# Kernel tuning notes

Measured on AMD Instinct MI355X. Metric: run time of the kernel, lower is better.

Reference implementation:

```python
import jax, jax.numpy as jnp
import numpy as np

N_NODES = 100000


def gcn_layer(x, row, col, ew, W, b, n_nodes):
    # PyG GCNConv: add self-loops (weight 1), symmetric normalization
    # deg^{-1/2}[row] * w * deg^{-1/2}[col], linear transform, scatter-add to col.
    loop = jnp.arange(n_nodes, dtype=row.dtype)
    row_f = jnp.concatenate([row, loop])
    col_f = jnp.concatenate([col, loop])
    ew_f = jnp.concatenate([ew, jnp.ones((n_nodes,), dtype=ew.dtype)])
    deg = jax.ops.segment_sum(ew_f, col_f, num_segments=n_nodes)  # [N]
    dinv = jnp.where(deg > 0, jax.lax.rsqrt(deg), 0.0)
    norm = dinv[row_f] * ew_f * dinv[col_f]  # [E+N]
    h = x @ W  # [N, F_out]
    msg = norm[:, None] * h[row_f]  # [E+N, F_out]
    out = jax.ops.segment_sum(msg, col_f, num_segments=n_nodes)
    return out + b


def setup_inputs() -> dict:
    key = jax.random.key(0)
    ks = jax.random.split(key, 6)
    n, e, d_in, d_h = N_NODES, 3200000, 128, 16
    x = jax.random.normal(ks[0], (n, d_in), dtype=jnp.float32)
    edge_index = jax.random.randint(ks[1], (2, e), 0, n, dtype=jnp.int64)
    edge_weight = jax.random.uniform(ks[2], (e,), dtype=jnp.float32)
    W1 = jax.random.normal(ks[3], (d_in, d_h), dtype=jnp.float32) * (1.0 / np.sqrt(d_in))
    b1 = jnp.zeros((d_h,), dtype=jnp.float32)
    W2 = jax.random.normal(ks[4], (d_h, 1), dtype=jnp.float32) * (1.0 / np.sqrt(d_h))
    b2 = jnp.zeros((1,), dtype=jnp.float32)
    return {"x": x, "edge_index": edge_index, "edge_weight": edge_weight,
            "W1": W1, "b1": b1, "W2": W2, "b2": b2}


def reference(x, edge_index, edge_weight, W1, b1, W2, b2):
    row, col = edge_index[0], edge_index[1]
    n = x.shape[0]
    h = gcn_layer(x, row, col, edge_weight, W1, b1, n)
    h = jax.nn.relu(h)
    out = gcn_layer(h, row, col, edge_weight, W2, b2, n)
    return out.squeeze(-1)  # [N]
```

## Files before the change

### kernel.cpp

```cpp
#include <hip/hip_runtime.h>


#define DH 16

__global__ void k_hist(const int* __restrict__ col, int* __restrict__ cnt, int E) {
    int e = blockIdx.x * blockDim.x + threadIdx.x;
    if (e < E) atomicAdd(&cnt[col[e]], 1);
}

__global__ __launch_bounds__(256) void k_scan1(const int* __restrict__ cnt,
                                               int* __restrict__ rowptr,
                                               int* __restrict__ blocksum, int N) {
    __shared__ int s[256];
    int i = blockIdx.x * 256 + threadIdx.x;
    int v = (i < N) ? cnt[i] : 0;
    s[threadIdx.x] = v;
    __syncthreads();
    for (int off = 1; off < 256; off <<= 1) {
        int t = (threadIdx.x >= off) ? s[threadIdx.x - off] : 0;
        __syncthreads();
        s[threadIdx.x] += t;
        __syncthreads();
    }
    if (i < N) rowptr[i] = s[threadIdx.x];
    if (threadIdx.x == 255) blocksum[blockIdx.x] = s[255];
}

__global__ __launch_bounds__(512) void k_scan2(int* __restrict__ blocksum, int nb) {
    __shared__ int s[512];
    int t = threadIdx.x;
    int v = (t < nb) ? blocksum[t] : 0;
    s[t] = v;
    __syncthreads();
    for (int off = 1; off < 512; off <<= 1) {
        int u = (t >= off) ? s[t - off] : 0;
        __syncthreads();
        s[t] += u;
        __syncthreads();
    }
    if (t < nb) blocksum[t] = s[t] - v;
}

__global__ void k_scan3(const int* __restrict__ cnt, int* __restrict__ rowptr,
                        const int* __restrict__ blocksum, int* __restrict__ cursor,
                        int N, int E) {
    int i = blockIdx.x * 256 + threadIdx.x;
    if (i < N) {
        int ex = blocksum[blockIdx.x] + rowptr[i] - cnt[i];
        rowptr[i] = ex;
        cursor[i] = ex;
    }
    if (i == 0) rowptr[N] = E;
}

__global__ void k_scatter(const int* __restrict__ row, const int* __restrict__ col,
                          const float* __restrict__ ew, int* __restrict__ cursor,
                          uint2* __restrict__ edata, int E) {
    int e = blockIdx.x * blockDim.x + threadIdx.x;
    if (e >= E) return;
    int slot = atomicAdd(&cursor[col[e]], 1);
    edata[slot] = make_uint2((unsigned)row[e], __float_as_uint(ew[e]));
}

__global__ __launch_bounds__(256) void k_degcsr(const int* __restrict__ rowptr,
                                                const uint2* __restrict__ edata,
                                                float* __restrict__ dinv, int N) {
    int node = (blockIdx.x * 256 + threadIdx.x) >> 6;
    if (node >= N) return;
    int lane = threadIdx.x & 63;
    int base = rowptr[node], end = rowptr[node + 1];
    float s = 0.f;
    for (int i = base + lane; i < end; i += 64) s += __uint_as_float(edata[i].y);
    #pragma unroll
    for (int m = 1; m < 64; m <<= 1) s += __shfl_xor(s, m, 64);
    if (lane == 0) dinv[node] = rsqrtf(s + 1.0f);
}

__global__ __launch_bounds__(256) void k_h1(const float* __restrict__ x,
                                            const float* __restrict__ W1,
                                            float* __restrict__ h) {
    __shared__ float Ws[128 * DH];
    __shared__ float xs[16 * 132];
    const int t = threadIdx.x;
    const int node0 = blockIdx.x * 16;

    #pragma unroll
    for (int i = 0; i < 8; ++i) Ws[t + 256 * i] = W1[t + 256 * i];

    const float4* xg = (const float4*)(x + (size_t)node0 * 128);
    #pragma unroll
    for (int it = 0; it < 2; ++it) {
        int idx = t + 256 * it;
        int n = idx >> 5, k4 = idx & 31;
        float4 v = xg[n * 32 + k4];
        *(float4*)(&xs[n * 132 + k4 * 4]) = v;
    }
    __syncthreads();

    const int node = t >> 4, feat = t & 15;
    const float* xr = &xs[node * 132];
    float acc = 0.f;
    #pragma unroll 8
    for (int k = 0; k < 128; ++k) acc += xr[k] * Ws[k * DH + feat];
    h[(size_t)(node0 + node) * DH + feat] = acc;
}

__global__ __launch_bounds__(256) void k_gather1(
    const int* __restrict__ rowptr, const uint2* __restrict__ edata,
    const float* __restrict__ dinv, const float* __restrict__ h,
    const float* __restrict__ b1, const float* __restrict__ W2,
    float* __restrict__ q, int N) {
    int node = (blockIdx.x * 256 + threadIdx.x) >> 6;
    if (node >= N) return;
    int lane = threadIdx.x & 63;
    int feat = lane & 15, g = lane >> 4;
    int base = rowptr[node], end = rowptr[node + 1];
    float acc = 0.f;
    for (int i = base + g; i < end; i += 4) {
        uint2 ed = edata[i];
        int r = ed.x;
        float w = __uint_as_float(ed.y);
        acc += dinv[r] * w * h[(size_t)r * DH + feat];
    }
    acc += __shfl_xor(acc, 16, 64);
    acc += __shfl_xor(acc, 32, 64);
    float dc = dinv[node];
    float ag = dc * acc + dc * dc * h[(size_t)node * DH + feat];
    float t = fmaxf(ag + b1[feat], 0.f) * W2[feat];
    t += __shfl_xor(t, 1, 64);
    t += __shfl_xor(t, 2, 64);
    t += __shfl_xor(t, 4, 64);
    t += __shfl_xor(t, 8, 64);
    if (lane == 0) q[node] = dc * t;
}

__global__ __launch_bounds__(256) void k_gather2(
    const int* __restrict__ rowptr, const uint2* __restrict__ edata,
    const float* __restrict__ dinv, const float* __restrict__ q,
    const float* __restrict__ b2, float* __restrict__ out, int N) {
    int node = (blockIdx.x * 256 + threadIdx.x) >> 6;
    if (node >= N) return;
    int lane = threadIdx.x & 63;
    int base = rowptr[node], end = rowptr[node + 1];
    float acc = 0.f;
    for (int i = base + lane; i < end; i += 64) {
        uint2 ed = edata[i];
        acc += __uint_as_float(ed.y) * q[ed.x];
    }
    #pragma unroll
    for (int m = 1; m < 64; m <<= 1) acc += __shfl_xor(acc, m, 64);
    if (lane == 0) out[node] = b2[0] + dinv[node] * (acc + q[node]);
}

extern "C" void kernel_launch(void* const* d_in, const int* in_sizes, int n_in,
                              void* d_out, int out_size, void* d_ws, size_t ws_size,
                              hipStream_t stream) {
    const float* x  = (const float*)d_in[0];
    const int*   ei = (const int*)d_in[1];
    const float* ew = (const float*)d_in[2];
    const float* W1 = (const float*)d_in[3];
    const float* b1 = (const float*)d_in[4];
    const float* W2 = (const float*)d_in[5];
    const float* b2 = (const float*)d_in[6];
    float* out = (float*)d_out;

    const int N = in_sizes[0] / 128;
    const int E = in_sizes[2];
    const int* row = ei;
    const int* col = ei + E;

    int* cnt      = (int*)d_ws;
    int* rowptr   = cnt + N;
    int* cursor   = rowptr + N + 1;
    int* blocksum = cursor + N;
    float* dinv   = (float*)(blocksum + 512);
    float* h      = dinv + N;
    float* q      = h + (size_t)16 * N;
    uintptr_t ep  = (uintptr_t)(q + N);
    ep = (ep + 7) & ~(uintptr_t)7;
    uint2* edata  = (uint2*)ep;

    const int eb = (E + 255) / 256;
    const int G1 = (N + 255) / 256;
    const int nodeb = (N * 64 + 255) / 256;

    hipMemsetAsync(cnt, 0, (size_t)N * sizeof(int), stream);
    k_hist<<<eb, 256, 0, stream>>>(col, cnt, E);
    k_scan1<<<G1, 256, 0, stream>>>(cnt, rowptr, blocksum, N);
    k_scan2<<<1, 512, 0, stream>>>(blocksum, G1);
    k_scan3<<<G1, 256, 0, stream>>>(cnt, rowptr, blocksum, cursor, N, E);
    k_scatter<<<eb, 256, 0, stream>>>(row, col, ew, cursor, edata, E);
    k_degcsr<<<nodeb, 256, 0, stream>>>(rowptr, edata, dinv, N);
    k_h1<<<N / 16, 256, 0, stream>>>(x, W1, h);
    k_gather1<<<nodeb, 256, 0, stream>>>(rowptr, edata, dinv, h, b1, W2, q, N);
    k_gather2<<<nodeb, 256, 0, stream>>>(rowptr, edata, dinv, q, b2, out, N);
}
```

Before: 641.0 us.

## Replace per-node CSR with 128-node bucket partitioning and shared-memory accumulation

Edges are no longer sorted into an exact per-node CSR. They are bucketed by destination into groups of 128 nodes, using block-local shared-memory histograms and one global cursor atomic per bucket, with the local node index packed into the high bits of the row id. Degree and both aggregation passes then run one block per bucket and accumulate into shared memory with LDS atomics. This removes the per-edge global atomics and the multi-pass scan, but adds shared-memory atomic contention and assumes row ids fit in 20 bits and NB is at most 784.

```diff
diff --git a/kernel.cpp b/kernel.cpp
--- a/kernel.cpp
+++ b/kernel.cpp
@@ -2,78 +2,111 @@
 
 
 #define DH 16
-
-__global__ void k_hist(const int* __restrict__ col, int* __restrict__ cnt, int E) {
-    int e = blockIdx.x * blockDim.x + threadIdx.x;
-    if (e < E) atomicAdd(&cnt[col[e]], 1);
-}
-
-__global__ __launch_bounds__(256) void k_scan1(const int* __restrict__ cnt,
-                                               int* __restrict__ rowptr,
-                                               int* __restrict__ blocksum, int N) {
-    __shared__ int s[256];
-    int i = blockIdx.x * 256 + threadIdx.x;
-    int v = (i < N) ? cnt[i] : 0;
-    s[threadIdx.x] = v;
-    __syncthreads();
-    for (int off = 1; off < 256; off <<= 1) {
-        int t = (threadIdx.x >= off) ? s[threadIdx.x - off] : 0;
-        __syncthreads();
-        s[threadIdx.x] += t;
-        __syncthreads();
-    }
-    if (i < N) rowptr[i] = s[threadIdx.x];
-    if (threadIdx.x == 255) blocksum[blockIdx.x] = s[255];
-}
-
-__global__ __launch_bounds__(512) void k_scan2(int* __restrict__ blocksum, int nb) {
-    __shared__ int s[512];
-    int t = threadIdx.x;
-    int v = (t < nb) ? blocksum[t] : 0;
+#define BSH 7
+#define BNODES 128
+#define NB_MAX 784
+#define CHUNK 4096
+
+__global__ __launch_bounds__(256) void k_Ahist(const int* __restrict__ col,
+                                               int* __restrict__ gCnt, int E, int NB) {
+    __shared__ int lh[NB_MAX];
+    const int tid = threadIdx.x;
+    for (int i = tid; i < NB; i += 256) lh[i] = 0;
+    __syncthreads();
+    const int base = blockIdx.x * CHUNK;
+    #pragma unroll
+    for (int k = 0; k < 16; ++k) {
+        int e = base + tid + 256 * k;
+        if (e < E) atomicAdd(&lh[col[e] >> BSH], 1);
+    }
+    __syncthreads();
+    for (int i = tid; i < NB; i += 256) {
+        int v = lh[i];
+        if (v) atomicAdd(&gCnt[i], v);
+    }
+}
+
+__global__ __launch_bounds__(1024) void k_Ascan(const int* __restrict__ gCnt,
+                                                int* __restrict__ gBase,
+                                                int* __restrict__ gCursor,
+                                                int NB, int E) {
+    __shared__ int s[1024];
+    const int t = threadIdx.x;
+    int v = (t < NB) ? gCnt[t] : 0;
     s[t] = v;
     __syncthreads();
-    for (int off = 1; off < 512; off <<= 1) {
+    for (int off = 1; off < 1024; off <<= 1) {
         int u = (t >= off) ? s[t - off] : 0;
         __syncthreads();
         s[t] += u;
         __syncthreads();
     }
-    if (t < nb) blocksum[t] = s[t] - v;
-}
-
-__global__ void k_scan3(const int* __restrict__ cnt, int* __restrict__ rowptr,
-                        const int* __restrict__ blocksum, int* __restrict__ cursor,
-                        int N, int E) {
-    int i = blockIdx.x * 256 + threadIdx.x;
-    if (i < N) {
-        int ex = blocksum[blockIdx.x] + rowptr[i] - cnt[i];
-        rowptr[i] = ex;
-        cursor[i] = ex;
-    }
-    if (i == 0) rowptr[N] = E;
-}
-
-__global__ void k_scatter(const int* __restrict__ row, const int* __restrict__ col,
-                          const float* __restrict__ ew, int* __restrict__ cursor,
-                          uint2* __restrict__ edata, int E) {
-    int e = blockIdx.x * blockDim.x + threadIdx.x;
-    if (e >= E) return;
-    int slot = atomicAdd(&cursor[col[e]], 1);
-    edata[slot] = make_uint2((unsigned)row[e], __float_as_uint(ew[e]));
-}
-
-__global__ __launch_bounds__(256) void k_degcsr(const int* __restrict__ rowptr,
-                                                const uint2* __restrict__ edata,
-                                                float* __restrict__ dinv, int N) {
-    int node = (blockIdx.x * 256 + threadIdx.x) >> 6;
-    if (node >= N) return;
-    int lane = threadIdx.x & 63;
-    int base = rowptr[node], end = rowptr[node + 1];
-    float s = 0.f;
-    for (int i = base + lane; i < end; i += 64) s += __uint_as_float(edata[i].y);
-    #pragma unroll
-    for (int m = 1; m < 64; m <<= 1) s += __shfl_xor(s, m, 64);
-    if (lane == 0) dinv[node] = rsqrtf(s + 1.0f);
+    if (t < NB) {
+        int ex = s[t] - v;
+        gBase[t] = ex;
+        gCursor[t] = ex;
+    }
+    if (t == 0) gBase[NB] = E;
+}
+
+__global__ __launch_bounds__(256) void k_Ascatter(const int* __restrict__ row,
+                                                  const int* __restrict__ col,
+                                                  const float* __restrict__ ew,
+                                                  int* __restrict__ gCursor,
+                                                  uint2* __restrict__ edata,
+                                                  int E, int NB) {
+    __shared__ int lh[NB_MAX], lbase[NB_MAX], lcur[NB_MAX];
+    const int tid = threadIdx.x;
+    for (int i = tid; i < NB; i += 256) lh[i] = 0;
+    __syncthreads();
+    const int base = blockIdx.x * CHUNK;
+    int r_[16], c_[16];
+    float w_[16];
+    #pragma unroll
+    for (int k = 0; k < 16; ++k) {
+        int e = base + tid + 256 * k;
+        bool ok = e < E;
+        c_[k] = ok ? col[e] : -1;
+        r_[k] = ok ? row[e] : 0;
+        w_[k] = ok ? ew[e] : 0.f;
+        if (ok) atomicAdd(&lh[c_[k] >> BSH], 1);
+    }
+    __syncthreads();
+    for (int b = tid; b < NB; b += 256) {
+        int v = lh[b];
+        if (v) {
+            lbase[b] = atomicAdd(&gCursor[b], v);
+            lcur[b] = 0;
+        }
+    }
+    __syncthreads();
+    #pragma unroll
+    for (int k = 0; k < 16; ++k) {
+        if (c_[k] >= 0) {
+            int b = c_[k] >> BSH;
+            int rem = c_[k] & (BNODES - 1);
+            int off = atomicAdd(&lcur[b], 1);
+            edata[lbase[b] + off] =
+                make_uint2((unsigned)r_[k] | ((unsigned)rem << 20), __float_as_uint(w_[k]));
+        }
+    }
+}
+
+__global__ __launch_bounds__(256) void k_deg(const int* __restrict__ gBase,
+                                             const uint2* __restrict__ edata,
+                                             float* __restrict__ dinv, int N) {
+    __shared__ float dg[BNODES];
+    const int tid = threadIdx.x;
+    if (tid < BNODES) dg[tid] = 0.f;
+    __syncthreads();
+    const int s = gBase[blockIdx.x], e = gBase[blockIdx.x + 1];
+    for (int i = s + tid; i < e; i += 256) {
+        uint2 ed = edata[i];
+        atomicAdd(&dg[ed.x >> 20], __uint_as_float(ed.y));
+    }
+    __syncthreads();
+    int node = (blockIdx.x << BSH) + tid;
+    if (tid < BNODES && node < N) dinv[node] = rsqrtf(dg[tid] + 1.0f);
 }
 
 __global__ __launch_bounds__(256) void k_h1(const float* __restrict__ x,
@@ -83,10 +116,8 @@
     __shared__ float xs[16 * 132];
     const int t = threadIdx.x;
     const int node0 = blockIdx.x * 16;
-
     #pragma unroll
     for (int i = 0; i < 8; ++i) Ws[t + 256 * i] = W1[t + 256 * i];
-
     const float4* xg = (const float4*)(x + (size_t)node0 * 128);
     #pragma unroll
     for (int it = 0; it < 2; ++it) {
@@ -96,7 +127,6 @@
         *(float4*)(&xs[n * 132 + k4 * 4]) = v;
     }
     __syncthreads();
-
     const int node = t >> 4, feat = t & 15;
     const float* xr = &xs[node * 132];
     float acc = 0.f;
@@ -106,50 +136,57 @@
 }
 
 __global__ __launch_bounds__(256) void k_gather1(
-    const int* __restrict__ rowptr, const uint2* __restrict__ edata,
+    const int* __restrict__ gBase, const uint2* __restrict__ edata,
     const float* __restrict__ dinv, const float* __restrict__ h,
     const float* __restrict__ b1, const float* __restrict__ W2,
     float* __restrict__ q, int N) {
-    int node = (blockIdx.x * 256 + threadIdx.x) >> 6;
-    if (node >= N) return;
-    int lane = threadIdx.x & 63;
-    int feat = lane & 15, g = lane >> 4;
-    int base = rowptr[node], end = rowptr[node + 1];
-    float acc = 0.f;
-    for (int i = base + g; i < end; i += 4) {
+    __shared__ float acc[DH][BNODES + 1];
+    __shared__ float b1s[DH], W2s[DH];
+    const int tid = threadIdx.x;
+    if (tid < DH) { b1s[tid] = b1[tid]; W2s[tid] = W2[tid]; }
+    for (int i = tid; i < DH * (BNODES + 1); i += 256) ((float*)acc)[i] = 0.f;
+    __syncthreads();
+    const int s = gBase[blockIdx.x], e = gBase[blockIdx.x + 1];
+    const int g = tid >> 4, f = tid & 15;
+    for (int i = s + g; i < e; i += 16) {
         uint2 ed = edata[i];
-        int r = ed.x;
+        int r = ed.x & 0xFFFFF;
+        int rem = ed.x >> 20;
         float w = __uint_as_float(ed.y);
-        acc += dinv[r] * w * h[(size_t)r * DH + feat];
-    }
-    acc += __shfl_xor(acc, 16, 64);
-    acc += __shfl_xor(acc, 32, 64);
-    float dc = dinv[node];
-    float ag = dc * acc + dc * dc * h[(size_t)node * DH + feat];
-    float t = fmaxf(ag + b1[feat], 0.f) * W2[feat];
-    t += __shfl_xor(t, 1, 64);
-    t += __shfl_xor(t, 2, 64);
-    t += __shfl_xor(t, 4, 64);
-    t += __shfl_xor(t, 8, 64);
-    if (lane == 0) q[node] = dc * t;
+        atomicAdd(&acc[f][rem], w * dinv[r] * h[r * DH + f]);
+    }
+    __syncthreads();
+    int node = (blockIdx.x << BSH) + tid;
+    if (tid < BNODES && node < N) {
+        float dc = dinv[node];
+        float t = 0.f;
+        #pragma unroll
+        for (int ff = 0; ff < DH; ++ff) {
+            float ag = dc * acc[ff][tid] + dc * dc * h[node * DH + ff];
+            t += fmaxf(ag + b1s[ff], 0.f) * W2s[ff];
+        }
+        q[node] = dc * t;
+    }
 }
 
 __global__ __launch_bounds__(256) void k_gather2(
-    const int* __restrict__ rowptr, const uint2* __restrict__ edata,
+    const int* __restrict__ gBase, const uint2* __restrict__ edata,
     const float* __restrict__ dinv, const float* __restrict__ q,
     const float* __restrict__ b2, float* __restrict__ out, int N) {
-    int node = (blockIdx.x * 256 + threadIdx.x) >> 6;
-    if (node >= N) return;
-    int lane = threadIdx.x & 63;
-    int base = rowptr[node], end = rowptr[node + 1];
-    float acc = 0.f;
-    for (int i = base + lane; i < end; i += 64) {
+    __shared__ float a2[BNODES];
+    const int tid = threadIdx.x;
+    if (tid < BNODES) a2[tid] = 0.f;
+    __syncthreads();
+    const int s = gBase[blockIdx.x], e = gBase[blockIdx.x + 1];
+    for (int i = s + tid; i < e; i += 256) {
         uint2 ed = edata[i];
-        acc += __uint_as_float(ed.y) * q[ed.x];
-    }
-    #pragma unroll
-    for (int m = 1; m < 64; m <<= 1) acc += __shfl_xor(acc, m, 64);
-    if (lane == 0) out[node] = b2[0] + dinv[node] * (acc + q[node]);
+        int r = ed.x & 0xFFFFF;
+        atomicAdd(&a2[ed.x >> 20], __uint_as_float(ed.y) * q[r]);
+    }
+    __syncthreads();
+    int node = (blockIdx.x << BSH) + tid;
+    if (tid < BNODES && node < N)
+        out[node] = b2[0] + dinv[node] * (a2[tid] + q[node]);
 }
 
 extern "C" void kernel_launch(void* const* d_in, const int* in_sizes, int n_in,
@@ -168,30 +205,26 @@
     const int E = in_sizes[2];
     const int* row = ei;
     const int* col = ei + E;
-
-    int* cnt      = (int*)d_ws;
-    int* rowptr   = cnt + N;
-    int* cursor   = rowptr + N + 1;
-    int* blocksum = cursor + N;
-    float* dinv   = (float*)(blocksum + 512);
-    float* h      = dinv + N;
-    float* q      = h + (size_t)16 * N;
-    uintptr_t ep  = (uintptr_t)(q + N);
+    const int NB = (N + BNODES - 1) >> BSH;
+
+    int* gCnt    = (int*)d_ws;
+    int* gBase   = gCnt + NB;
+    int* gCursor = gBase + NB + 1;
+    float* dinv  = (float*)(gCursor + NB);
+    float* h     = dinv + N;
+    float* q     = h + (size_t)16 * N;
+    uintptr_t ep = (uintptr_t)(q + N);
     ep = (ep + 7) & ~(uintptr_t)7;
-    uint2* edata  = (uint2*)ep;
-
-    const int eb = (E + 255) / 256;
-    const int G1 = (N + 255) / 256;
-    const int nodeb = (N * 64 + 255) / 256;
-
-    hipMemsetAsync(cnt, 0, (size_t)N * sizeof(int), stream);
-    k_hist<<<eb, 256, 0, stream>>>(col, cnt, E);
-    k_scan1<<<G1, 256, 0, stream>>>(cnt, rowptr, blocksum, N);
-    k_scan2<<<1, 512, 0, stream>>>(blocksum, G1);
-    k_scan3<<<G1, 256, 0, stream>>>(cnt, rowptr, blocksum, cursor, N, E);
-    k_scatter<<<eb, 256, 0, stream>>>(row, col, ew, cursor, edata, E);
-    k_degcsr<<<nodeb, 256, 0, stream>>>(rowptr, edata, dinv, N);
+    uint2* edata = (uint2*)ep;
+
+    const int ablocks = (E + CHUNK - 1) / CHUNK;
+
+    hipMemsetAsync(gCnt, 0, (size_t)NB * sizeof(int), stream);
+    k_Ahist<<<ablocks, 256, 0, stream>>>(col, gCnt, E, NB);
+    k_Ascan<<<1, 1024, 0, stream>>>(gCnt, gBase, gCursor, NB, E);
+    k_Ascatter<<<ablocks, 256, 0, stream>>>(row, col, ew, gCursor, edata, E, NB);
+    k_deg<<<NB, 256, 0, stream>>>(gBase, edata, dinv, N);
     k_h1<<<N / 16, 256, 0, stream>>>(x, W1, h);
-    k_gather1<<<nodeb, 256, 0, stream>>>(rowptr, edata, dinv, h, b1, W2, q, N);
-    k_gather2<<<nodeb, 256, 0, stream>>>(rowptr, edata, dinv, q, b2, out, N);
-}
+    k_gather1<<<NB, 256, 0, stream>>>(gBase, edata, dinv, h, b1, W2, q, N);
+    k_gather2<<<NB, 256, 0, stream>>>(gBase, edata, dinv, q, b2, out, N);
+}
```

After: 589.9 us. -8.0%, faster.
